# Kernel tuning notes

Measured on AMD Instinct MI355X. Metric: run time of the kernel, lower is better.

Reference implementation:

```python
import jax, jax.numpy as jnp
import numpy as np

L, D, H, V, S, HID = 4, 1024, 16, 32000, 2048, 2816
HD = D // H  # 64
EPS = 1e-5


def setup_inputs() -> dict:
    key = jax.random.key(0)
    ks = jax.random.split(key, 10)
    s = 0.02  # init scale for numerical sanity; math is unaffected
    return {
        "tokens": jax.random.randint(ks[0], (1, S), 0, V),
        "emb": jax.random.normal(ks[1], (V, D), jnp.float32) * s,
        "wq": jax.random.normal(ks[2], (L, D, D), jnp.float32) * s,
        "wk": jax.random.normal(ks[3], (L, D, D), jnp.float32) * s,
        "wv": jax.random.normal(ks[4], (L, D, D), jnp.float32) * s,
        "wo": jax.random.normal(ks[5], (L, D, D), jnp.float32) * s,
        "w1": jax.random.normal(ks[6], (L, HID, D), jnp.float32) * s,
        "w2": jax.random.normal(ks[7], (L, D, HID), jnp.float32) * s,
        "w3": jax.random.normal(ks[8], (L, HID, D), jnp.float32) * s,
        "attn_norm_w": jnp.ones((L, D), jnp.float32),
        "ffn_norm_w": jnp.ones((L, D), jnp.float32),
        "final_norm_w": jnp.ones((D,), jnp.float32),
    }


def _rmsnorm(x, w):
    return x * jax.lax.rsqrt(jnp.mean(x * x, axis=-1, keepdims=True) + EPS) * w


def _rope(x, cos, sin):
    # x: [B,S,H,HD]; interleaved pairs (..., -1, 2) as in apply_rotary_emb
    xr, xi = x[..., 0::2], x[..., 1::2]
    outr = xr * cos - xi * sin
    outi = xr * sin + xi * cos
    return jnp.stack([outr, outi], axis=-1).reshape(x.shape)


def reference(tokens, emb, wq, wk, wv, wo, w1, w2, w3, attn_norm_w, ffn_norm_w, final_norm_w):
    # precompute_freqs_cis(head_dim, seq)
    inv_freq = 1.0 / (10000.0 ** (jnp.arange(0, HD, 2, dtype=jnp.float32) / HD))
    fr = jnp.outer(jnp.arange(S, dtype=jnp.float32), inv_freq)  # [S, HD/2]
    cos = jnp.cos(fr)[None, :, None, :]
    sin = jnp.sin(fr)[None, :, None, :]
    mask = jnp.triu(jnp.full((S, S), -jnp.inf, jnp.float32), k=1)
    scale = 1.0 / jnp.sqrt(jnp.float32(HD))

    h = emb[tokens]  # [B,S,D] embedding lookup (dropout p=0 -> identity)
    B = h.shape[0]

    def block(h, p):
        Wq, Wk, Wv, Wo, W1, W2, W3, anw, fnw = p
        x = _rmsnorm(h, anw)
        q = (x @ Wq.T).reshape(B, S, H, HD)
        k = (x @ Wk.T).reshape(B, S, H, HD)
        v = (x @ Wv.T).reshape(B, S, H, HD)
        q = _rope(q, cos, sin)
        k = _rope(k, cos, sin)
        q, k, v = (t.transpose(0, 2, 1, 3) for t in (q, k, v))  # [B,H,S,HD]
        scores = jnp.einsum("bhqd,bhkd->bhqk", q, k) * scale + mask
        attn = jax.nn.softmax(scores, axis=-1)
        o = jnp.einsum("bhqk,bhkd->bhqd", attn, v)
        o = o.transpose(0, 2, 1, 3).reshape(B, S, D)
        h = h + o @ Wo.T
        y = _rmsnorm(h, fnw)
        ff = (jax.nn.silu(y @ W1.T) * (y @ W3.T)) @ W2.T
        return h + ff, None

    h, _ = jax.lax.scan(block, h, (wq, wk, wv, wo, w1, w2, w3, attn_norm_w, ffn_norm_w))
    h = _rmsnorm(h, final_norm_w)
    logits = h[:, -1:, :] @ emb.T  # output weight tied to tok_embeddings; last position only
    return logits
```

## Files before the change

### kernel.cpp

```cpp
#include <hip/hip_runtime.h>

#define LNUM 4
#define DIM 1024
#define NH 16
#define VOCAB 32000
#define SEQ 2048
#define HIDD 2816

typedef _Float16 f16;
typedef _Float16 h8_t __attribute__((ext_vector_type(8)));
typedef _Float16 h4_t __attribute__((ext_vector_type(4)));
typedef float f4_t __attribute__((ext_vector_type(4)));

#define MFMA(a, b, c) __builtin_amdgcn_mfma_f32_16x16x32_f16(a, b, c, 0, 0, 0)

__device__ __forceinline__ void async16(void* lds, const void* g) {
  __builtin_amdgcn_global_load_lds(
      (const __attribute__((address_space(1))) void*)g,
      (__attribute__((address_space(3))) void*)lds, 16, 0, 0);
}

template <int N>
__device__ __forceinline__ float ror16(float x) {
  int r = __builtin_amdgcn_update_dpp(0, __builtin_bit_cast(int, x),
                                      0x120 | N, 0xF, 0xF, true);
  return __builtin_bit_cast(float, r);
}
__device__ __forceinline__ float rmax16(float v) {
  v = fmaxf(v, ror16<1>(v));
  v = fmaxf(v, ror16<2>(v));
  v = fmaxf(v, ror16<4>(v));
  v = fmaxf(v, ror16<8>(v));
  return v;
}
__device__ __forceinline__ float rsum16(float v) {
  v += ror16<1>(v);
  v += ror16<2>(v);
  v += ror16<4>(v);
  v += ror16<8>(v);
  return v;
}
__device__ __forceinline__ float qswap(float x) {
  int r = __builtin_amdgcn_update_dpp(0, __builtin_bit_cast(int, x), 0xB1,
                                      0xF, 0xF, true);
  return __builtin_bit_cast(float, r);
}

__global__ __launch_bounds__(256) void cast_layer_k(
    const float* __restrict__ wq, const float* __restrict__ wk,
    const float* __restrict__ wv, const float* __restrict__ wo,
    const float* __restrict__ w1, const float* __restrict__ w3,
    const float* __restrict__ w2, f16* __restrict__ wqkv,
    f16* __restrict__ wod, f16* __restrict__ w13, f16* __restrict__ w2d) {
  const int DD4c = DIM * DIM / 4, HD4c = HIDD * DIM / 4;
  int i = blockIdx.x * 256 + threadIdx.x;
  const float* s;
  f16* d;
  int si, di;
  if (i < 3 * DD4c) {
    d = wqkv;
    di = i;
    if (i < DD4c) {
      s = wq; si = i;
    } else if (i < 2 * DD4c) {
      s = wk; si = i - DD4c;
    } else {
      s = wv; si = i - 2 * DD4c;
    }
  } else if (i < 4 * DD4c) {
    s = wo; si = i - 3 * DD4c; d = wod; di = si;
  } else if (i < 4 * DD4c + HD4c) {
    s = w1; si = i - 4 * DD4c; d = w13; di = si;
  } else if (i < 4 * DD4c + 2 * HD4c) {
    s = w3; si = i - 4 * DD4c - HD4c; d = w13; di = si + HD4c;
  } else {
    s = w2; si = i - 4 * DD4c - 2 * HD4c; d = w2d; di = si;
  }
  float4 v = ((const float4*)s)[si];
  ((h4_t*)d)[di] = (h4_t){(f16)v.x, (f16)v.y, (f16)v.z, (f16)v.w};
}

__global__ __launch_bounds__(256) void embed_k(const int* __restrict__ tok,
                                               const float* __restrict__ emb,
                                               float* __restrict__ h) {
  const int s = blockIdx.x, t = threadIdx.x;
  ((float4*)(h + (size_t)s * DIM))[t] =
      ((const float4*)(emb + (size_t)tok[s] * DIM))[t];
}

__global__ void rope_tab_k(float* __restrict__ tab) {
  int i = blockIdx.x * 256 + threadIdx.x;
  if (i >= SEQ * 32) return;
  int s = i >> 5, f = i & 31;
  float inv = powf(10000.f, -(float)f * (1.f / 32.f));
  float a = (float)s * inv;
  float sn, c;
  sincosf(a, &sn, &c);
  tab[i * 2] = c;
  tab[i * 2 + 1] = sn;
}

__global__ __launch_bounds__(256) void rmsnorm_k(const float* __restrict__ h,
                                                 const float* __restrict__ w,
                                                 f16* __restrict__ out) {
  const int s = blockIdx.x, t = threadIdx.x;
  float4 v = ((const float4*)(h + (size_t)s * DIM))[t];
  float ss = v.x * v.x + v.y * v.y + v.z * v.z + v.w * v.w;
#pragma unroll
  for (int d = 1; d < 64; d <<= 1) ss += __shfl_xor(ss, d);
  __shared__ float red[4];
  if ((t & 63) == 0) red[t >> 6] = ss;
  __syncthreads();
  float tot = red[0] + red[1] + red[2] + red[3];
  float sc = rsqrtf(tot * (1.f / (float)DIM) + 1e-5f);
  float4 wv = ((const float4*)w)[t];
  ((h4_t*)(out + (size_t)s * DIM))[t] =
      (h4_t){(f16)(v.x * sc * wv.x), (f16)(v.y * sc * wv.y),
             (f16)(v.z * sc * wv.z), (f16)(v.w * sc * wv.w)};
}

__global__ __launch_bounds__(256) void rmsnorm_sk(float* __restrict__ h,
                                                  const float* __restrict__ p,
                                                  const float* __restrict__ w,
                                                  f16* __restrict__ out) {
  const int s = blockIdx.x, t = threadIdx.x;
  float4 v = ((const float4*)(h + (size_t)s * DIM))[t];
  float4 a = ((const float4*)(p + (size_t)s * DIM))[t];
  float4 b = ((const float4*)(p + (size_t)SEQ * DIM + (size_t)s * DIM))[t];
  v.x += a.x + b.x;
  v.y += a.y + b.y;
  v.z += a.z + b.z;
  v.w += a.w + b.w;
  ((float4*)(h + (size_t)s * DIM))[t] = v;
  float ss = v.x * v.x + v.y * v.y + v.z * v.z + v.w * v.w;
#pragma unroll
  for (int d = 1; d < 64; d <<= 1) ss += __shfl_xor(ss, d);
  __shared__ float red[4];
  if ((t & 63) == 0) red[t >> 6] = ss;
  __syncthreads();
  float tot = red[0] + red[1] + red[2] + red[3];
  float sc = rsqrtf(tot * (1.f / (float)DIM) + 1e-5f);
  float4 wv = ((const float4*)w)[t];
  ((h4_t*)(out + (size_t)s * DIM))[t] =
      (h4_t){(f16)(v.x * sc * wv.x), (f16)(v.y * sc * wv.y),
             (f16)(v.z * sc * wv.z), (f16)(v.w * sc * wv.w)};
}

__global__ __launch_bounds__(256) void final_norm_sk(
    const float* __restrict__ h, const float* __restrict__ p,
    const float* __restrict__ w, float* __restrict__ hn) {
  const int t = threadIdx.x;
  const size_t row = (size_t)(SEQ - 1) * DIM;
  float4 v = ((const float4*)(h + row))[t];
  float4 a = ((const float4*)(p + row))[t];
  float4 b = ((const float4*)(p + (size_t)SEQ * DIM + row))[t];
  v.x += a.x + b.x;
  v.y += a.y + b.y;
  v.z += a.z + b.z;
  v.w += a.w + b.w;
  float ss = v.x * v.x + v.y * v.y + v.z * v.z + v.w * v.w;
#pragma unroll
  for (int d = 1; d < 64; d <<= 1) ss += __shfl_xor(ss, d);
  __shared__ float red[4];
  if ((t & 63) == 0) red[t >> 6] = ss;
  __syncthreads();
  float tot = red[0] + red[1] + red[2] + red[3];
  float sc = rsqrtf(tot * (1.f / (float)DIM) + 1e-5f);
  float4 wv = ((const float4*)w)[t];
  ((float4*)hn)[t] = make_float4(v.x * sc * wv.x, v.y * sc * wv.y,
                                 v.z * sc * wv.z, v.w * sc * wv.w);
}

__global__ __launch_bounds__(256) void logits_k(const float* __restrict__ hn,
                                                const float* __restrict__ emb,
                                                float* __restrict__ out) {
  const int v = blockIdx.x * 4 + (threadIdx.x >> 6);
  const int lane = threadIdx.x & 63;
  const float4* er = (const float4*)(emb + (size_t)v * DIM);
  const float4* hr = (const float4*)hn;
  float s = 0.f;
#pragma unroll
  for (int i = 0; i < 4; i++) {
    float4 a = er[lane + i * 64];
    float4 b = hr[lane + i * 64];
    s += a.x * b.x + a.y * b.y + a.z * b.z + a.w * b.w;
  }
#pragma unroll
  for (int d = 1; d < 64; d <<= 1) s += __shfl_xor(s, d);
  if (lane == 0) out[v] = s;
}

__global__ __launch_bounds__(256) void silu_k(const f16* __restrict__ g13,
                                              f16* __restrict__ t) {
  int c = blockIdx.x * 256 + threadIdx.x;
  int s = blockIdx.y;
  float g = (float)g13[(size_t)s * (2 * HIDD) + c];
  float u = (float)g13[(size_t)s * (2 * HIDD) + HIDD + c];
  float r = g / (1.f + __expf(-g)) * u;
  t[(size_t)s * HIDD + c] = (f16)r;
}

__global__ __launch_bounds__(256) void transpose_v(const f16* __restrict__ qkv,
                                                   f16* __restrict__ vT) {
  __shared__ f16 tile[32][34];
  int bs = blockIdx.x * 32;
  int bc = blockIdx.y * 32;
  int tx = threadIdx.x & 31, ty = threadIdx.x >> 5;
#pragma unroll
  for (int i = ty; i < 32; i += 8)
    tile[i][tx] = qkv[(size_t)(bs + i) * 3072 + 2048 + bc + tx];
  __syncthreads();
#pragma unroll
  for (int i = ty; i < 32; i += 8)
    vT[(size_t)(bc + i) * SEQ + bs + tx] = tile[tx][i];
}


#define GEMM_PIPE_LOOP(KLEN, LDSTRIDE)                                       \
  {                                                                          \
    async16(lA, gA);                                                         \
    async16(lA + 64 * 32, gA + (size_t)64 * (LDSTRIDE));                     \
    async16(lB, gB);                                                         \
    async16(lB + 64 * 32, gB + (size_t)64 * (LDSTRIDE));                     \
    for (int k0 = 0; k0 < (KLEN); k0 += 32) {                                \
      const int cur = (k0 >> 5) & 1;                                         \
      if (k0 + 32 < (KLEN)) {                                                \
        const int nxt = cur ^ 1;                                             \
        async16(lA + nxt * 4096, gA + k0 + 32);                              \
        async16(lA + nxt * 4096 + 64 * 32,                                   \
                gA + (size_t)64 * (LDSTRIDE) + k0 + 32);                     \
        async16(lB + nxt * 4096, gB + k0 + 32);                              \
        async16(lB + nxt * 4096 + 64 * 32,                                   \
                gB + (size_t)64 * (LDSTRIDE) + k0 + 32);                     \
        asm volatile("s_waitcnt vmcnt(4)" ::: "memory");                     \
      } else {                                                               \
        asm volatile("s_waitcnt vmcnt(0)" ::: "memory");                     \
      }                                                                      \
      asm volatile("s_barrier" ::: "memory");                                \
      const f16* As_c = As + cur * 4096;                                     \
      const f16* Bs_c = Bs + cur * 4096;                                     \
      h8_t af[4], bfr[4];                                                    \
      _Pragma("unroll") for (int m = 0; m < 4; m++) af[m] =                  \
          *(const h8_t*)(As_c + (wr * 64 + m * 16 + lr) * 32 +               \
                         ((lk ^ sw) << 3));                                  \
      _Pragma("unroll") for (int n = 0; n < 4; n++) bfr[n] =                 \
          *(const h8_t*)(Bs_c + (wc * 64 + n * 16 + lr) * 32 +               \
                         ((lk ^ sw) << 3));                                  \
      _Pragma("unroll") for (int m = 0; m < 4; m++)                          \
          _Pragma("unroll") for (int n = 0; n < 4; n++) acc[m][n] =          \
              MFMA(af[m], bfr[n], acc[m][n]);                                \
      asm volatile("s_waitcnt lgkmcnt(0)" ::: "memory");                     \
      asm volatile("s_barrier" ::: "memory");                                \
    }                                                                        \
  }

template <int EPI>
__global__ __launch_bounds__(256) void gemm_bt(const f16* __restrict__ A,
                                               const f16* __restrict__ B,
                                               void* __restrict__ Cout, int M,
                                               int N, int K) {
  __shared__ __align__(16) f16 As[2 * 128 * 32];
  __shared__ __align__(16) f16 Bs[2 * 128 * 32];
  const int t = threadIdx.x;
  const int lane = t & 63;
  const int wave = t >> 6;
  const int wr = wave >> 1, wc = wave & 1;
  const int bm = blockIdx.x, bn = blockIdx.y;
  const int lr = lane & 15, lk = lane >> 4;
  const int sw = (lr >> 1) & 3;

  const int srow = t >> 2;
  const int scol = (((t & 3) ^ ((t >> 3) & 3))) * 8;
  const f16* gA = A + (size_t)(bm * 128 + srow) * K + scol;
  const f16* gB = B + (size_t)(bn * 128 + srow) * K + scol;
  f16* lA = As + t * 8;
  f16* lB = Bs + t * 8;

  f4_t acc[4][4];
#pragma unroll
  for (int m = 0; m < 4; m++)
#pragma unroll
    for (int n = 0; n < 4; n++) acc[m][n] = {0.f, 0.f, 0.f, 0.f};

  GEMM_PIPE_LOOP(K, K)

  const int orow = bm * 128 + wr * 64 + lk * 4;
  const int ocol = bn * 128 + wc * 64 + lr;
#pragma unroll
  for (int m = 0; m < 4; m++)
#pragma unroll
    for (int n = 0; n < 4; n++)
#pragma unroll
      for (int j = 0; j < 4; j++) {
        int r = orow + m * 16 + j;
        int c = ocol + n * 16;
        if (EPI == 0) {
          ((f16*)Cout)[(size_t)r * N + c] = (f16)acc[m][n][j];
        } else {
          float* pC = (float*)Cout + (size_t)r * N + c;
          *pC += acc[m][n][j];
        }
      }
}

__global__ __launch_bounds__(256) void gemm_qkv(const f16* __restrict__ A,
                                                const f16* __restrict__ B,
                                                f16* __restrict__ C,
                                                const float* __restrict__ tab) {
  const int N = 3 * DIM, K = DIM;
  __shared__ __align__(16) f16 As[2 * 128 * 32];
  __shared__ __align__(16) f16 Bs[2 * 128 * 32];
  const int t = threadIdx.x;
  const int lane = t & 63;
  const int wave = t >> 6;
  const int wr = wave >> 1, wc = wave & 1;
  const int bm = blockIdx.x, bn = blockIdx.y;
  const int lr = lane & 15, lk = lane >> 4;
  const int sw = (lr >> 1) & 3;

  const int srow = t >> 2;
  const int scol = (((t & 3) ^ ((t >> 3) & 3))) * 8;
  const f16* gA = A + (size_t)(bm * 128 + srow) * K + scol;
  const f16* gB = B + (size_t)(bn * 128 + srow) * K + scol;
  f16* lA = As + t * 8;
  f16* lB = Bs + t * 8;

  f4_t acc[4][4];
#pragma unroll
  for (int m = 0; m < 4; m++)
#pragma unroll
    for (int n = 0; n < 4; n++) acc[m][n] = {0.f, 0.f, 0.f, 0.f};

  GEMM_PIPE_LOOP(K, K)

  const int orow = bm * 128 + wr * 64 + lk * 4;
  const int ocol = bn * 128 + wc * 64 + lr;
  const float ssign = (lr & 1) ? 1.f : -1.f;
#pragma unroll
  for (int m = 0; m < 4; m++)
#pragma unroll
    for (int n = 0; n < 4; n++) {
      const int c = ocol + n * 16;
      const bool qk = c < 2048;
      const int f = (n * 16 + lr) >> 1;
#pragma unroll
      for (int j = 0; j < 4; j++) {
        int r = orow + m * 16 + j;
        float sv = acc[m][n][j];
        float pa = qswap(sv);
        if (qk) {
          float2 cs = ((const float2*)tab)[r * 32 + f];
          sv = sv * cs.x + pa * cs.y * ssign;
        }
        C[(size_t)r * N + c] = (f16)sv;
      }
    }
}

__global__ __launch_bounds__(256) void gemm_skp(const f16* __restrict__ A,
                                                const f16* __restrict__ B,
                                                float* __restrict__ Cp, int N,
                                                int ld, int Ks) {
  __shared__ __align__(16) f16 As[2 * 128 * 32];
  __shared__ __align__(16) f16 Bs[2 * 128 * 32];
  const int t = threadIdx.x;
  const int lane = t & 63;
  const int wave = t >> 6;
  const int wr = wave >> 1, wc = wave & 1;
  const int bm = blockIdx.x, bn = blockIdx.y, bk = blockIdx.z;
  const int lr = lane & 15, lk = lane >> 4;
  const int sw = (lr >> 1) & 3;

  const f16* Ao = A + (size_t)bk * Ks;
  const f16* Bo = B + (size_t)bk * Ks;
  float* Cout = Cp + (size_t)bk * gridDim.x * 128 * N;

  const int srow = t >> 2;
  const int scol = (((t & 3) ^ ((t >> 3) & 3))) * 8;
  const f16* gA = Ao + (size_t)(bm * 128 + srow) * ld + scol;
  const f16* gB = Bo + (size_t)(bn * 128 + srow) * ld + scol;
  f16* lA = As + t * 8;
  f16* lB = Bs + t * 8;

  f4_t acc[4][4];
#pragma unroll
  for (int m = 0; m < 4; m++)
#pragma unroll
    for (int n = 0; n < 4; n++) acc[m][n] = {0.f, 0.f, 0.f, 0.f};

  GEMM_PIPE_LOOP(Ks, ld)

  const int orow = bm * 128 + wr * 64 + lk * 4;
  const int ocol = bn * 128 + wc * 64 + lr;
#pragma unroll
  for (int m = 0; m < 4; m++)
#pragma unroll
    for (int n = 0; n < 4; n++)
#pragma unroll
      for (int j = 0; j < 4; j++)
        Cout[(size_t)(orow + m * 16 + j) * N + ocol + n * 16] = acc[m][n][j];
}

__global__ __launch_bounds__(256) void attn_k(const f16* __restrict__ qkv,
                                              const f16* __restrict__ vT,
                                              f16* __restrict__ o) {
  const int hh = blockIdx.x;
  const int qb2 = blockIdx.y;
  const int tid = threadIdx.x;
  const int wave = tid >> 6;
  const int lane = tid & 63;
  const int lr = lane & 15, lk = lane >> 4;
  __shared__ __align__(16) char P[4][4096];
  __shared__ float MBml[3][64][16];
  __shared__ f16 MBo[3][64][32];
  char* Pw = P[wave];

#pragma unroll 1
  for (int pass = 0; pass < 2; ++pass) {
    const int qb = pass ? qb2 : (63 - qb2);
    const int q0 = qb * 32;

    h8_t qf[2][2];
#pragma unroll
    for (int m = 0; m < 2; m++)
#pragma unroll
      for (int ks = 0; ks < 2; ks++)
        qf[m][ks] = *(const h8_t*)(qkv + (size_t)(q0 + m * 16 + lr) * 3072 +
                                   hh * 64 + ks * 32 + lk * 8);

    float mrow[2][4], lsum[2][4];
    f4_t oacc[2][4];
#pragma unroll
    for (int m = 0; m < 2; m++)
#pragma unroll
      for (int j = 0; j < 4; j++) {
        mrow[m][j] = -1e30f;
        lsum[m][j] = 0.f;
      }
#pragma unroll
    for (int m = 0; m < 2; m++)
#pragma unroll
      for (int n = 0; n < 4; n++) oacc[m][n] = {0.f, 0.f, 0.f, 0.f};

    const int ntiles = (qb >> 1) + 1;
    for (int kt = wave; kt < ntiles; kt += 4) {
      f4_t sacc[2][4];
#pragma unroll
      for (int m = 0; m < 2; m++)
#pragma unroll
        for (int n = 0; n < 4; n++) sacc[m][n] = {0.f, 0.f, 0.f, 0.f};
#pragma unroll
      for (int ks = 0; ks < 2; ks++) {
        h8_t kf[4];
#pragma unroll
        for (int n = 0; n < 4; n++)
          kf[n] = *(const h8_t*)(qkv + (size_t)(kt * 64 + n * 16 + lr) * 3072 +
                                 1024 + hh * 64 + ks * 32 + lk * 8);
#pragma unroll
        for (int m = 0; m < 2; m++)
#pragma unroll
          for (int n = 0; n < 4; n++)
            sacc[m][n] = MFMA(qf[m][ks], kf[n], sacc[m][n]);
      }
      const bool lastt = (kt == ntiles - 1);
      float pv[2][4][4];
#pragma unroll
      for (int m = 0; m < 2; m++)
#pragma unroll
        for (int n = 0; n < 4; n++)
#pragma unroll
          for (int j = 0; j < 4; j++) {
            float sv = sacc[m][n][j] * 0.125f;
            if (lastt && (kt * 64 + n * 16 + lr) > (q0 + m * 16 + lk * 4 + j))
              sv = -1e30f;
            pv[m][n][j] = sv;
          }
#pragma unroll
      for (int m = 0; m < 2; m++)
#pragma unroll
        for (int j = 0; j < 4; j++) {
          float mx = fmaxf(fmaxf(pv[m][0][j], pv[m][1][j]),
                           fmaxf(pv[m][2][j], pv[m][3][j]));
          mx = rmax16(mx);
          float mnew = fmaxf(mrow[m][j], mx);
          float corr = __expf(mrow[m][j] - mnew);
          mrow[m][j] = mnew;
          float rs = 0.f;
#pragma unroll
          for (int n = 0; n < 4; n++) {
            float pe = __expf(pv[m][n][j] - mnew);
            pv[m][n][j] = pe;
            rs += pe;
          }
          rs = rsum16(rs);
          lsum[m][j] = lsum[m][j] * corr + rs;
#pragma unroll
          for (int n = 0; n < 4; n++) oacc[m][n][j] *= corr;
        }
#pragma unroll
      for (int m = 0; m < 2; m++)
#pragma unroll
        for (int n = 0; n < 4; n++)
#pragma unroll
          for (int j = 0; j < 4; j++) {
            int r = m * 16 + lk * 4 + j, c = n * 16 + lr;
            int off = (r * 128 + c * 2) ^ ((r & 7) << 4);
            *(f16*)(Pw + off) = (f16)pv[m][n][j];
          }
#pragma unroll
      for (int ks = 0; ks < 2; ks++) {
        h8_t pf[2], vf[4];
#pragma unroll
        for (int m = 0; m < 2; m++) {
          int r = m * 16 + lr;
          int off = (r * 128 + ks * 64 + lk * 16) ^ ((r & 7) << 4);
          pf[m] = *(const h8_t*)(Pw + off);
        }
#pragma unroll
        for (int n = 0; n < 4; n++)
          vf[n] = *(const h8_t*)(vT + (size_t)(hh * 64 + n * 16 + lr) * SEQ +
                                 kt * 64 + ks * 32 + lk * 8);
#pragma unroll
        for (int m = 0; m < 2; m++)
#pragma unroll
          for (int n = 0; n < 4; n++)
            oacc[m][n] = MFMA(pf[m], vf[n], oacc[m][n]);
      }
    }

    if (wave > 0) {
      float* dml = &MBml[wave - 1][lane][0];
      f16* doo = &MBo[wave - 1][lane][0];
#pragma unroll
      for (int m = 0; m < 2; m++)
#pragma unroll
        for (int j = 0; j < 4; j++) {
          dml[m * 4 + j] = mrow[m][j];
          dml[8 + m * 4 + j] = lsum[m][j];
        }
#pragma unroll
      for (int m = 0; m < 2; m++)
#pragma unroll
        for (int n = 0; n < 4; n++)
#pragma unroll
          for (int j = 0; j < 4; j++)
            doo[m * 16 + n * 4 + j] = (f16)oacc[m][n][j];
    }
    __syncthreads();
    if (wave == 0) {
#pragma unroll
      for (int m = 0; m < 2; m++)
#pragma unroll
        for (int j = 0; j < 4; j++) {
          float M = mrow[m][j];
#pragma unroll
          for (int w = 0; w < 3; w++) M = fmaxf(M, MBml[w][lane][m * 4 + j]);
          float sc0 = __expf(mrow[m][j] - M);
          float L = lsum[m][j] * sc0;
          float scw[3];
#pragma unroll
          for (int w = 0; w < 3; w++) {
            scw[w] = __expf(MBml[w][lane][m * 4 + j] - M);
            L += MBml[w][lane][8 + m * 4 + j] * scw[w];
          }
          float invL = 1.f / L;
#pragma unroll
          for (int n = 0; n < 4; n++) {
            float val = oacc[m][n][j] * sc0;
#pragma unroll
            for (int w = 0; w < 3; w++)
              val += (float)MBo[w][lane][m * 16 + n * 4 + j] * scw[w];
            o[(size_t)(q0 + m * 16 + lk * 4 + j) * DIM + hh * 64 + n * 16 +
              lr] = (f16)(val * invL);
          }
        }
    }
    __syncthreads();
  }
}

extern "C" void kernel_launch(void* const* d_in, const int* in_sizes, int n_in,
                              void* d_out, int out_size, void* d_ws,
                              size_t ws_size, hipStream_t stream) {
  (void)in_sizes; (void)n_in; (void)out_size; (void)ws_size;
  const int* tokens = (const int*)d_in[0];
  const float* emb = (const float*)d_in[1];
  const float* wq = (const float*)d_in[2];
  const float* wk = (const float*)d_in[3];
  const float* wv = (const float*)d_in[4];
  const float* wo = (const float*)d_in[5];
  const float* w1 = (const float*)d_in[6];
  const float* w2 = (const float*)d_in[7];
  const float* w3 = (const float*)d_in[8];
  const float* anw = (const float*)d_in[9];
  const float* fnw = (const float*)d_in[10];
  const float* finw = (const float*)d_in[11];
  float* out = (float*)d_out;

  char* p = (char*)d_ws;
  auto alloc = [&](size_t bytes) {
    char* r = p;
    p += (bytes + 255) & ~(size_t)255;
    return r;
  };
  f16* wqkv_l = (f16*)alloc((size_t)3 * DIM * DIM * 2);
  f16* wo_l = (f16*)alloc((size_t)DIM * DIM * 2);
  f16* w13_l = (f16*)alloc((size_t)2 * HIDD * DIM * 2);
  f16* w2_l = (f16*)alloc((size_t)DIM * HIDD * 2);
  float* hbuf = (float*)alloc((size_t)SEQ * DIM * 4);
  f16* x_h = (f16*)alloc((size_t)SEQ * DIM * 2);
  f16* qkv_h = (f16*)alloc((size_t)SEQ * 3 * DIM * 2);
  f16* vT_h = (f16*)alloc((size_t)DIM * SEQ * 2);
  f16* o_h = (f16*)alloc((size_t)SEQ * DIM * 2);
  f16* g13_h = (f16*)alloc((size_t)SEQ * 2 * HIDD * 2);
  f16* t_h = (f16*)alloc((size_t)SEQ * HIDD * 2);
  float* skbuf = (float*)alloc((size_t)2 * SEQ * DIM * 4);
  float* tab = (float*)alloc((size_t)SEQ * 32 * 2 * 4);
  float* hn = (float*)alloc(4096);

  embed_k<<<SEQ, 256, 0, stream>>>(tokens, emb, hbuf);
  rope_tab_k<<<(SEQ * 32 + 255) / 256, 256, 0, stream>>>(tab);

  const int CAST_BLOCKS = (4 * (DIM * DIM / 4) + 3 * (HIDD * DIM / 4)) / 256;
  for (int l = 0; l < LNUM; l++) {
    const size_t offDD = (size_t)l * DIM * DIM;
    const size_t offHD = (size_t)l * HIDD * DIM;
    cast_layer_k<<<CAST_BLOCKS, 256, 0, stream>>>(
        wq + offDD, wk + offDD, wv + offDD, wo + offDD, w1 + offHD,
        w3 + offHD, w2 + offHD, wqkv_l, wo_l, w13_l, w2_l);

    if (l == 0) {
      rmsnorm_k<<<SEQ, 256, 0, stream>>>(hbuf, anw, x_h);
    } else {
      rmsnorm_sk<<<SEQ, 256, 0, stream>>>(hbuf, skbuf, anw + (size_t)l * DIM,
                                          x_h);
    }
    {
      dim3 g(SEQ / 128, (3 * DIM) / 128);
      gemm_qkv<<<g, 256, 0, stream>>>(x_h, wqkv_l, qkv_h, tab);
    }
    {
      dim3 g(SEQ / 32, DIM / 32);
      transpose_v<<<g, 256, 0, stream>>>(qkv_h, vT_h);
    }
    {
      dim3 g(NH, SEQ / 64);
      attn_k<<<g, 256, 0, stream>>>(qkv_h, vT_h, o_h);
    }
    {
      dim3 g(SEQ / 128, DIM / 128, 2);
      gemm_skp<<<g, 256, 0, stream>>>(o_h, wo_l, skbuf, DIM, DIM, DIM / 2);
    }
    rmsnorm_sk<<<SEQ, 256, 0, stream>>>(hbuf, skbuf, fnw + (size_t)l * DIM,
                                        x_h);
    {
      dim3 g(SEQ / 128, (2 * HIDD) / 128);
      gemm_bt<0><<<g, 256, 0, stream>>>(x_h, w13_l, g13_h, SEQ, 2 * HIDD, DIM);
    }
    {
      dim3 g(HIDD / 256, SEQ);
      silu_k<<<g, 256, 0, stream>>>(g13_h, t_h);
    }
    {
      dim3 g(SEQ / 128, DIM / 128, 2);
      gemm_skp<<<g, 256, 0, stream>>>(t_h, w2_l, skbuf, DIM, HIDD, HIDD / 2);
    }
  }
  final_norm_sk<<<1, 256, 0, stream>>>(hbuf, skbuf, finw, hn);
  logits_k<<<VOCAB / 4, 256, 0, stream>>>(hn, emb, out);
}
```

Measured before the change: 808.4 us.

## Fuse V transpose and SwiGLU into GEMM epilogues, rebalance attention grid

The V-projection transpose now happens in the QKV GEMM epilogue, which writes vT directly. W1 and W3 rows are interleaved in pairs during the weight cast, so the W13 GEMM can compute silu(g)*u with a lane swap and write the hidden activation directly. This removes the transpose_v and silu_k kernels and the g13 buffer round trip. Attention now launches one 32-row query block per workgroup instead of two paired passes, and it rescales the running max only when the new max grows by more than 8, which skips most correction multiplies at some numerical risk.

```diff
diff --git a/kernel.cpp b/kernel.cpp
--- a/kernel.cpp
+++ b/kernel.cpp
@@ -70,9 +70,11 @@
   } else if (i < 4 * DD4c) {
     s = wo; si = i - 3 * DD4c; d = wod; di = si;
   } else if (i < 4 * DD4c + HD4c) {
-    s = w1; si = i - 4 * DD4c; d = w13; di = si;
+    s = w1; si = i - 4 * DD4c; d = w13;
+    di = ((si >> 8) << 9) + (si & 255);
   } else if (i < 4 * DD4c + 2 * HD4c) {
-    s = w3; si = i - 4 * DD4c - HD4c; d = w13; di = si + HD4c;
+    s = w3; si = i - 4 * DD4c - HD4c; d = w13;
+    di = ((si >> 8) << 9) + 256 + (si & 255);
   } else {
     s = w2; si = i - 4 * DD4c - 2 * HD4c; d = w2d; di = si;
   }
@@ -189,32 +191,6 @@
   for (int d = 1; d < 64; d <<= 1) s += __shfl_xor(s, d);
   if (lane == 0) out[v] = s;
 }
-
-__global__ __launch_bounds__(256) void silu_k(const f16* __restrict__ g13,
-                                              f16* __restrict__ t) {
-  int c = blockIdx.x * 256 + threadIdx.x;
-  int s = blockIdx.y;
-  float g = (float)g13[(size_t)s * (2 * HIDD) + c];
-  float u = (float)g13[(size_t)s * (2 * HIDD) + HIDD + c];
-  float r = g / (1.f + __expf(-g)) * u;
-  t[(size_t)s * HIDD + c] = (f16)r;
-}
-
-__global__ __launch_bounds__(256) void transpose_v(const f16* __restrict__ qkv,
-                                                   f16* __restrict__ vT) {
-  __shared__ f16 tile[32][34];
-  int bs = blockIdx.x * 32;
-  int bc = blockIdx.y * 32;
-  int tx = threadIdx.x & 31, ty = threadIdx.x >> 5;
-#pragma unroll
-  for (int i = ty; i < 32; i += 8)
-    tile[i][tx] = qkv[(size_t)(bs + i) * 3072 + 2048 + bc + tx];
-  __syncthreads();
-#pragma unroll
-  for (int i = ty; i < 32; i += 8)
-    vT[(size_t)(bc + i) * SEQ + bs + tx] = tile[tx][i];
-}
-
 
 #define GEMM_PIPE_LOOP(KLEN, LDSTRIDE)                                       \
   {                                                                          \
@@ -254,83 +230,34 @@
     }                                                                        \
   }
 
-template <int EPI>
-__global__ __launch_bounds__(256) void gemm_bt(const f16* __restrict__ A,
-                                               const f16* __restrict__ B,
-                                               void* __restrict__ Cout, int M,
-                                               int N, int K) {
-  __shared__ __align__(16) f16 As[2 * 128 * 32];
-  __shared__ __align__(16) f16 Bs[2 * 128 * 32];
-  const int t = threadIdx.x;
-  const int lane = t & 63;
-  const int wave = t >> 6;
-  const int wr = wave >> 1, wc = wave & 1;
-  const int bm = blockIdx.x, bn = blockIdx.y;
-  const int lr = lane & 15, lk = lane >> 4;
-  const int sw = (lr >> 1) & 3;
-
-  const int srow = t >> 2;
-  const int scol = (((t & 3) ^ ((t >> 3) & 3))) * 8;
-  const f16* gA = A + (size_t)(bm * 128 + srow) * K + scol;
-  const f16* gB = B + (size_t)(bn * 128 + srow) * K + scol;
-  f16* lA = As + t * 8;
-  f16* lB = Bs + t * 8;
-
-  f4_t acc[4][4];
-#pragma unroll
-  for (int m = 0; m < 4; m++)
-#pragma unroll
-    for (int n = 0; n < 4; n++) acc[m][n] = {0.f, 0.f, 0.f, 0.f};
-
-  GEMM_PIPE_LOOP(K, K)
-
-  const int orow = bm * 128 + wr * 64 + lk * 4;
-  const int ocol = bn * 128 + wc * 64 + lr;
-#pragma unroll
-  for (int m = 0; m < 4; m++)
-#pragma unroll
-    for (int n = 0; n < 4; n++)
-#pragma unroll
-      for (int j = 0; j < 4; j++) {
-        int r = orow + m * 16 + j;
-        int c = ocol + n * 16;
-        if (EPI == 0) {
-          ((f16*)Cout)[(size_t)r * N + c] = (f16)acc[m][n][j];
-        } else {
-          float* pC = (float*)Cout + (size_t)r * N + c;
-          *pC += acc[m][n][j];
-        }
-      }
-}
+#define GEMM_PREAMBLE(BPTR, KSTRIDE)                                         \
+  const int t = threadIdx.x;                                                 \
+  const int lane = t & 63;                                                   \
+  const int wave = t >> 6;                                                   \
+  const int wr = wave >> 1, wc = wave & 1;                                   \
+  const int bm = blockIdx.x, bn = blockIdx.y;                                \
+  const int lr = lane & 15, lk = lane >> 4;                                  \
+  const int sw = (lr >> 1) & 3;                                              \
+  const int srow = t >> 2;                                                   \
+  const int scol = (((t & 3) ^ ((t >> 3) & 3))) * 8;                         \
+  const f16* gA = A + (size_t)(bm * 128 + srow) * (KSTRIDE) + scol;          \
+  const f16* gB = (BPTR) + (size_t)(bn * 128 + srow) * (KSTRIDE) + scol;     \
+  f16* lA = As + t * 8;                                                      \
+  f16* lB = Bs + t * 8;                                                      \
+  f4_t acc[4][4];                                                            \
+  _Pragma("unroll") for (int m = 0; m < 4; m++)                              \
+      _Pragma("unroll") for (int n = 0; n < 4; n++) acc[m][n] = {0.f, 0.f,   \
+                                                                 0.f, 0.f};
 
 __global__ __launch_bounds__(256) void gemm_qkv(const f16* __restrict__ A,
                                                 const f16* __restrict__ B,
                                                 f16* __restrict__ C,
+                                                f16* __restrict__ vT,
                                                 const float* __restrict__ tab) {
   const int N = 3 * DIM, K = DIM;
   __shared__ __align__(16) f16 As[2 * 128 * 32];
   __shared__ __align__(16) f16 Bs[2 * 128 * 32];
-  const int t = threadIdx.x;
-  const int lane = t & 63;
-  const int wave = t >> 6;
-  const int wr = wave >> 1, wc = wave & 1;
-  const int bm = blockIdx.x, bn = blockIdx.y;
-  const int lr = lane & 15, lk = lane >> 4;
-  const int sw = (lr >> 1) & 3;
-
-  const int srow = t >> 2;
-  const int scol = (((t & 3) ^ ((t >> 3) & 3))) * 8;
-  const f16* gA = A + (size_t)(bm * 128 + srow) * K + scol;
-  const f16* gB = B + (size_t)(bn * 128 + srow) * K + scol;
-  f16* lA = As + t * 8;
-  f16* lB = Bs + t * 8;
-
-  f4_t acc[4][4];
-#pragma unroll
-  for (int m = 0; m < 4; m++)
-#pragma unroll
-    for (int n = 0; n < 4; n++) acc[m][n] = {0.f, 0.f, 0.f, 0.f};
-
+  GEMM_PREAMBLE(B, K)
   GEMM_PIPE_LOOP(K, K)
 
   const int orow = bm * 128 + wr * 64 + lk * 4;
@@ -341,241 +268,251 @@
 #pragma unroll
     for (int n = 0; n < 4; n++) {
       const int c = ocol + n * 16;
-      const bool qk = c < 2048;
       const int f = (n * 16 + lr) >> 1;
-#pragma unroll
-      for (int j = 0; j < 4; j++) {
-        int r = orow + m * 16 + j;
-        float sv = acc[m][n][j];
-        float pa = qswap(sv);
-        if (qk) {
+      if (c < 2048) {
+#pragma unroll
+        for (int j = 0; j < 4; j++) {
+          int r = orow + m * 16 + j;
+          float sv = acc[m][n][j];
+          float pa = qswap(sv);
           float2 cs = ((const float2*)tab)[r * 32 + f];
           sv = sv * cs.x + pa * cs.y * ssign;
-        }
-        C[(size_t)r * N + c] = (f16)sv;
+          C[(size_t)r * N + c] = (f16)sv;
+        }
+      } else {
+        h4_t pack;
+#pragma unroll
+        for (int j = 0; j < 4; j++) pack[j] = (f16)acc[m][n][j];
+        *(h4_t*)(vT + (size_t)(c - 2048) * SEQ + orow + m * 16) = pack;
       }
     }
 }
 
+__global__ __launch_bounds__(256) void gemm_w13i(const f16* __restrict__ A,
+                                                 const f16* __restrict__ B,
+                                                 f16* __restrict__ T) {
+  const int K = DIM;
+  __shared__ __align__(16) f16 As[2 * 128 * 32];
+  __shared__ __align__(16) f16 Bs[2 * 128 * 32];
+  GEMM_PREAMBLE(B, K)
+  GEMM_PIPE_LOOP(K, K)
+
+  const int orow = bm * 128 + wr * 64 + lk * 4;
+  const int ocol = bn * 128 + wc * 64 + lr;
+  const bool even = (lr & 1) == 0;
+#pragma unroll
+  for (int m = 0; m < 4; m++)
+#pragma unroll
+    for (int n = 0; n < 4; n++) {
+      const int h = (ocol + n * 16) >> 1;
+#pragma unroll
+      for (int j = 0; j < 4; j++) {
+        float g = acc[m][n][j];
+        float u = qswap(g);
+        float r = g / (1.f + __expf(-g)) * u;
+        if (even)
+          T[(size_t)(orow + m * 16 + j) * HIDD + h] = (f16)r;
+      }
+    }
+}
+
 __global__ __launch_bounds__(256) void gemm_skp(const f16* __restrict__ A,
-                                                const f16* __restrict__ B,
+                                                const f16* __restrict__ B0,
                                                 float* __restrict__ Cp, int N,
                                                 int ld, int Ks) {
   __shared__ __align__(16) f16 As[2 * 128 * 32];
   __shared__ __align__(16) f16 Bs[2 * 128 * 32];
-  const int t = threadIdx.x;
-  const int lane = t & 63;
-  const int wave = t >> 6;
-  const int wr = wave >> 1, wc = wave & 1;
-  const int bm = blockIdx.x, bn = blockIdx.y, bk = blockIdx.z;
-  const int lr = lane & 15, lk = lane >> 4;
-  const int sw = (lr >> 1) & 3;
-
-  const f16* Ao = A + (size_t)bk * Ks;
-  const f16* Bo = B + (size_t)bk * Ks;
-  float* Cout = Cp + (size_t)bk * gridDim.x * 128 * N;
-
-  const int srow = t >> 2;
-  const int scol = (((t & 3) ^ ((t >> 3) & 3))) * 8;
-  const f16* gA = Ao + (size_t)(bm * 128 + srow) * ld + scol;
-  const f16* gB = Bo + (size_t)(bn * 128 + srow) * ld + scol;
-  f16* lA = As + t * 8;
-  f16* lB = Bs + t * 8;
-
-  f4_t acc[4][4];
-#pragma unroll
-  for (int m = 0; m < 4; m++)
-#pragma unroll
-    for (int n = 0; n < 4; n++) acc[m][n] = {0.f, 0.f, 0.f, 0.f};
-
-  GEMM_PIPE_LOOP(Ks, ld)
-
-  const int orow = bm * 128 + wr * 64 + lk * 4;
-  const int ocol = bn * 128 + wc * 64 + lr;
-#pragma unroll
-  for (int m = 0; m < 4; m++)
-#pragma unroll
-    for (int n = 0; n < 4; n++)
-#pragma unroll
-      for (int j = 0; j < 4; j++)
-        Cout[(size_t)(orow + m * 16 + j) * N + ocol + n * 16] = acc[m][n][j];
+  const int bk = blockIdx.z;
+  const f16* Aof = A + (size_t)bk * Ks;
+  const f16* B = B0 + (size_t)bk * Ks;
+  {
+    const f16* A = Aof;
+    GEMM_PREAMBLE(B, ld)
+    GEMM_PIPE_LOOP(Ks, ld)
+
+    float* Cout = Cp + (size_t)bk * gridDim.x * 128 * N;
+    const int orow = bm * 128 + wr * 64 + lk * 4;
+    const int ocol = bn * 128 + wc * 64 + lr;
+#pragma unroll
+    for (int m = 0; m < 4; m++)
+#pragma unroll
+      for (int n = 0; n < 4; n++)
+#pragma unroll
+        for (int j = 0; j < 4; j++)
+          Cout[(size_t)(orow + m * 16 + j) * N + ocol + n * 16] =
+              acc[m][n][j];
+  }
 }
 
 __global__ __launch_bounds__(256) void attn_k(const f16* __restrict__ qkv,
                                               const f16* __restrict__ vT,
                                               f16* __restrict__ o) {
   const int hh = blockIdx.x;
-  const int qb2 = blockIdx.y;
+  const int qb = 63 - blockIdx.y;
   const int tid = threadIdx.x;
   const int wave = tid >> 6;
   const int lane = tid & 63;
   const int lr = lane & 15, lk = lane >> 4;
+  const int q0 = qb * 32;
   __shared__ __align__(16) char P[4][4096];
   __shared__ float MBml[3][64][16];
   __shared__ f16 MBo[3][64][32];
   char* Pw = P[wave];
 
-#pragma unroll 1
-  for (int pass = 0; pass < 2; ++pass) {
-    const int qb = pass ? qb2 : (63 - qb2);
-    const int q0 = qb * 32;
-
-    h8_t qf[2][2];
+  h8_t qf[2][2];
+#pragma unroll
+  for (int m = 0; m < 2; m++)
+#pragma unroll
+    for (int ks = 0; ks < 2; ks++)
+      qf[m][ks] = *(const h8_t*)(qkv + (size_t)(q0 + m * 16 + lr) * 3072 +
+                                 hh * 64 + ks * 32 + lk * 8);
+
+  float mrow[2][4], lsum[2][4];
+  f4_t oacc[2][4];
+#pragma unroll
+  for (int m = 0; m < 2; m++)
+#pragma unroll
+    for (int j = 0; j < 4; j++) {
+      mrow[m][j] = -1e30f;
+      lsum[m][j] = 0.f;
+    }
+#pragma unroll
+  for (int m = 0; m < 2; m++)
+#pragma unroll
+    for (int n = 0; n < 4; n++) oacc[m][n] = {0.f, 0.f, 0.f, 0.f};
+
+  const int ntiles = (qb >> 1) + 1;
+  for (int kt = wave; kt < ntiles; kt += 4) {
+    f4_t sacc[2][4];
 #pragma unroll
     for (int m = 0; m < 2; m++)
 #pragma unroll
-      for (int ks = 0; ks < 2; ks++)
-        qf[m][ks] = *(const h8_t*)(qkv + (size_t)(q0 + m * 16 + lr) * 3072 +
-                                   hh * 64 + ks * 32 + lk * 8);
-
-    float mrow[2][4], lsum[2][4];
-    f4_t oacc[2][4];
+      for (int n = 0; n < 4; n++) sacc[m][n] = {0.f, 0.f, 0.f, 0.f};
+#pragma unroll
+    for (int ks = 0; ks < 2; ks++) {
+      h8_t kf[4];
+#pragma unroll
+      for (int n = 0; n < 4; n++)
+        kf[n] = *(const h8_t*)(qkv + (size_t)(kt * 64 + n * 16 + lr) * 3072 +
+                               1024 + hh * 64 + ks * 32 + lk * 8);
+#pragma unroll
+      for (int m = 0; m < 2; m++)
+#pragma unroll
+        for (int n = 0; n < 4; n++)
+          sacc[m][n] = MFMA(qf[m][ks], kf[n], sacc[m][n]);
+    }
+    const bool lastt = (kt == ntiles - 1);
+    float pv[2][4][4];
 #pragma unroll
     for (int m = 0; m < 2; m++)
 #pragma unroll
+      for (int n = 0; n < 4; n++)
+#pragma unroll
+        for (int j = 0; j < 4; j++) {
+          float sv = sacc[m][n][j] * 0.125f;
+          if (lastt && (kt * 64 + n * 16 + lr) > (q0 + m * 16 + lk * 4 + j))
+            sv = -1e30f;
+          pv[m][n][j] = sv;
+        }
+#pragma unroll
+    for (int m = 0; m < 2; m++)
+#pragma unroll
       for (int j = 0; j < 4; j++) {
-        mrow[m][j] = -1e30f;
-        lsum[m][j] = 0.f;
+        float mx = fmaxf(fmaxf(pv[m][0][j], pv[m][1][j]),
+                         fmaxf(pv[m][2][j], pv[m][3][j]));
+        mx = rmax16(mx);
+        if (mx > mrow[m][j] + 8.f) {
+          float corr = __expf(mrow[m][j] - mx);
+          lsum[m][j] *= corr;
+#pragma unroll
+          for (int n = 0; n < 4; n++) oacc[m][n][j] *= corr;
+          mrow[m][j] = mx;
+        }
+        float rs = 0.f;
+#pragma unroll
+        for (int n = 0; n < 4; n++) {
+          float pe = __expf(pv[m][n][j] - mrow[m][j]);
+          pv[m][n][j] = pe;
+          rs += pe;
+        }
+        rs = rsum16(rs);
+        lsum[m][j] += rs;
       }
 #pragma unroll
     for (int m = 0; m < 2; m++)
 #pragma unroll
-      for (int n = 0; n < 4; n++) oacc[m][n] = {0.f, 0.f, 0.f, 0.f};
-
-    const int ntiles = (qb >> 1) + 1;
-    for (int kt = wave; kt < ntiles; kt += 4) {
-      f4_t sacc[2][4];
+      for (int n = 0; n < 4; n++)
+#pragma unroll
+        for (int j = 0; j < 4; j++) {
+          int r = m * 16 + lk * 4 + j, c = n * 16 + lr;
+          int off = (r * 128 + c * 2) ^ ((r & 7) << 4);
+          *(f16*)(Pw + off) = (f16)pv[m][n][j];
+        }
+#pragma unroll
+    for (int ks = 0; ks < 2; ks++) {
+      h8_t pf[2], vf[4];
+#pragma unroll
+      for (int m = 0; m < 2; m++) {
+        int r = m * 16 + lr;
+        int off = (r * 128 + ks * 64 + lk * 16) ^ ((r & 7) << 4);
+        pf[m] = *(const h8_t*)(Pw + off);
+      }
+#pragma unroll
+      for (int n = 0; n < 4; n++)
+        vf[n] = *(const h8_t*)(vT + (size_t)(hh * 64 + n * 16 + lr) * SEQ +
+                               kt * 64 + ks * 32 + lk * 8);
 #pragma unroll
       for (int m = 0; m < 2; m++)
 #pragma unroll
-        for (int n = 0; n < 4; n++) sacc[m][n] = {0.f, 0.f, 0.f, 0.f};
-#pragma unroll
-      for (int ks = 0; ks < 2; ks++) {
-        h8_t kf[4];
-#pragma unroll
         for (int n = 0; n < 4; n++)
-          kf[n] = *(const h8_t*)(qkv + (size_t)(kt * 64 + n * 16 + lr) * 3072 +
-                                 1024 + hh * 64 + ks * 32 + lk * 8);
-#pragma unroll
-        for (int m = 0; m < 2; m++)
-#pragma unroll
-          for (int n = 0; n < 4; n++)
-            sacc[m][n] = MFMA(qf[m][ks], kf[n], sacc[m][n]);
+          oacc[m][n] = MFMA(pf[m], vf[n], oacc[m][n]);
+    }
+  }
+
+  if (wave > 0) {
+    float* dml = &MBml[wave - 1][lane][0];
+    f16* doo = &MBo[wave - 1][lane][0];
+#pragma unroll
+    for (int m = 0; m < 2; m++)
+#pragma unroll
+      for (int j = 0; j < 4; j++) {
+        dml[m * 4 + j] = mrow[m][j];
+        dml[8 + m * 4 + j] = lsum[m][j];
+        float inv = lsum[m][j] > 0.f ? 1.f / lsum[m][j] : 0.f;
+#pragma unroll
+        for (int n = 0; n < 4; n++)
+          doo[m * 16 + n * 4 + j] = (f16)(oacc[m][n][j] * inv);
       }
-      const bool lastt = (kt == ntiles - 1);
-      float pv[2][4][4];
-#pragma unroll
-      for (int m = 0; m < 2; m++)
-#pragma unroll
-        for (int n = 0; n < 4; n++)
-#pragma unroll
-          for (int j = 0; j < 4; j++) {
-            float sv = sacc[m][n][j] * 0.125f;
-            if (lastt && (kt * 64 + n * 16 + lr) > (q0 + m * 16 + lk * 4 + j))
-              sv = -1e30f;
-            pv[m][n][j] = sv;
-          }
-#pragma unroll
-      for (int m = 0; m < 2; m++)
-#pragma unroll
-        for (int j = 0; j < 4; j++) {
-          float mx = fmaxf(fmaxf(pv[m][0][j], pv[m][1][j]),
-                           fmaxf(pv[m][2][j], pv[m][3][j]));
-          mx = rmax16(mx);
-          float mnew = fmaxf(mrow[m][j], mx);
-          float corr = __expf(mrow[m][j] - mnew);
-          mrow[m][j] = mnew;
-          float rs = 0.f;
-#pragma unroll
-          for (int n = 0; n < 4; n++) {
-            float pe = __expf(pv[m][n][j] - mnew);
-            pv[m][n][j] = pe;
-            rs += pe;
-          }
-          rs = rsum16(rs);
-          lsum[m][j] = lsum[m][j] * corr + rs;
-#pragma unroll
-          for (int n = 0; n < 4; n++) oacc[m][n][j] *= corr;
-        }
-#pragma unroll
-      for (int m = 0; m < 2; m++)
-#pragma unroll
-        for (int n = 0; n < 4; n++)
-#pragma unroll
-          for (int j = 0; j < 4; j++) {
-            int r = m * 16 + lk * 4 + j, c = n * 16 + lr;
-            int off = (r * 128 + c * 2) ^ ((r & 7) << 4);
-            *(f16*)(Pw + off) = (f16)pv[m][n][j];
-          }
-#pragma unroll
-      for (int ks = 0; ks < 2; ks++) {
-        h8_t pf[2], vf[4];
-#pragma unroll
-        for (int m = 0; m < 2; m++) {
-          int r = m * 16 + lr;
-          int off = (r * 128 + ks * 64 + lk * 16) ^ ((r & 7) << 4);
-          pf[m] = *(const h8_t*)(Pw + off);
-        }
-#pragma unroll
-        for (int n = 0; n < 4; n++)
-          vf[n] = *(const h8_t*)(vT + (size_t)(hh * 64 + n * 16 + lr) * SEQ +
-                                 kt * 64 + ks * 32 + lk * 8);
-#pragma unroll
-        for (int m = 0; m < 2; m++)
-#pragma unroll
-          for (int n = 0; n < 4; n++)
-            oacc[m][n] = MFMA(pf[m], vf[n], oacc[m][n]);
+  }
+  __syncthreads();
+  if (wave == 0) {
+#pragma unroll
+    for (int m = 0; m < 2; m++)
+#pragma unroll
+      for (int j = 0; j < 4; j++) {
+        float M = mrow[m][j];
+#pragma unroll
+        for (int w = 0; w < 3; w++) M = fmaxf(M, MBml[w][lane][m * 4 + j]);
+        float e0 = __expf(mrow[m][j] - M);
+        float L = lsum[m][j] * e0;
+        float wt[3];
+#pragma unroll
+        for (int w = 0; w < 3; w++) {
+          wt[w] = MBml[w][lane][8 + m * 4 + j] *
+                  __expf(MBml[w][lane][m * 4 + j] - M);
+          L += wt[w];
+        }
+        float invL = 1.f / L;
+#pragma unroll
+        for (int n = 0; n < 4; n++) {
+          float val = oacc[m][n][j] * e0;
+#pragma unroll
+          for (int w = 0; w < 3; w++)
+            val += (float)MBo[w][lane][m * 16 + n * 4 + j] * wt[w];
+          o[(size_t)(q0 + m * 16 + lk * 4 + j) * DIM + hh * 64 + n * 16 +
+            lr] = (f16)(val * invL);
+        }
       }
-    }
-
-    if (wave > 0) {
-      float* dml = &MBml[wave - 1][lane][0];
-      f16* doo = &MBo[wave - 1][lane][0];
-#pragma unroll
-      for (int m = 0; m < 2; m++)
-#pragma unroll
-        for (int j = 0; j < 4; j++) {
-          dml[m * 4 + j] = mrow[m][j];
-          dml[8 + m * 4 + j] = lsum[m][j];
-        }
-#pragma unroll
-      for (int m = 0; m < 2; m++)
-#pragma unroll
-        for (int n = 0; n < 4; n++)
-#pragma unroll
-          for (int j = 0; j < 4; j++)
-            doo[m * 16 + n * 4 + j] = (f16)oacc[m][n][j];
-    }
-    __syncthreads();
-    if (wave == 0) {
-#pragma unroll
-      for (int m = 0; m < 2; m++)
-#pragma unroll
-        for (int j = 0; j < 4; j++) {
-          float M = mrow[m][j];
-#pragma unroll
-          for (int w = 0; w < 3; w++) M = fmaxf(M, MBml[w][lane][m * 4 + j]);
-          float sc0 = __expf(mrow[m][j] - M);
-          float L = lsum[m][j] * sc0;
-          float scw[3];
-#pragma unroll
-          for (int w = 0; w < 3; w++) {
-            scw[w] = __expf(MBml[w][lane][m * 4 + j] - M);
-            L += MBml[w][lane][8 + m * 4 + j] * scw[w];
-          }
-          float invL = 1.f / L;
-#pragma unroll
-          for (int n = 0; n < 4; n++) {
-            float val = oacc[m][n][j] * sc0;
-#pragma unroll
-            for (int w = 0; w < 3; w++)
-              val += (float)MBo[w][lane][m * 16 + n * 4 + j] * scw[w];
-            o[(size_t)(q0 + m * 16 + lk * 4 + j) * DIM + hh * 64 + n * 16 +
-              lr] = (f16)(val * invL);
-          }
-        }
-    }
-    __syncthreads();
   }
 }
 
@@ -612,7 +549,6 @@
   f16* qkv_h = (f16*)alloc((size_t)SEQ * 3 * DIM * 2);
   f16* vT_h = (f16*)alloc((size_t)DIM * SEQ * 2);
   f16* o_h = (f16*)alloc((size_t)SEQ * DIM * 2);
-  f16* g13_h = (f16*)alloc((size_t)SEQ * 2 * HIDD * 2);
   f16* t_h = (f16*)alloc((size_t)SEQ * HIDD * 2);
   float* skbuf = (float*)alloc((size_t)2 * SEQ * DIM * 4);
   float* tab = (float*)alloc((size_t)SEQ * 32 * 2 * 4);
@@ -637,14 +573,10 @@
     }
     {
       dim3 g(SEQ / 128, (3 * DIM) / 128);
-      gemm_qkv<<<g, 256, 0, stream>>>(x_h, wqkv_l, qkv_h, tab);
+      gemm_qkv<<<g, 256, 0, stream>>>(x_h, wqkv_l, qkv_h, vT_h, tab);
     }
     {
-      dim3 g(SEQ / 32, DIM / 32);
-      transpose_v<<<g, 256, 0, stream>>>(qkv_h, vT_h);
-    }
-    {
-      dim3 g(NH, SEQ / 64);
+      dim3 g(NH, SEQ / 32);
       attn_k<<<g, 256, 0, stream>>>(qkv_h, vT_h, o_h);
     }
     {
@@ -655,11 +587,7 @@
                                         x_h);
     {
       dim3 g(SEQ / 128, (2 * HIDD) / 128);
-      gemm_bt<0><<<g, 256, 0, stream>>>(x_h, w13_l, g13_h, SEQ, 2 * HIDD, DIM);
-    }
-    {
-      dim3 g(HIDD / 256, SEQ);
-      silu_k<<<g, 256, 0, stream>>>(g13_h, t_h);
+      gemm_w13i<<<g, 256, 0, stream>>>(x_h, w13_l, t_h);
     }
     {
       dim3 g(SEQ / 128, DIM / 128, 2);
```

New measurement: 775.0 us. 1.04x faster.
